# Performance work log

Measured on AMD Instinct MI355X. Metric: run time of the kernel, lower is better.

## Reference

```python
import jax, jax.numpy as jnp
import numpy as np

B, N, E, F, C = 4, 10000, 160000, 128, 128
NUM_ITERATIONS = 3  # num_iterations init arg


def setup_inputs() -> dict:
    key = jax.random.key(0)
    ks = jax.random.split(key, 8)
    objects = jax.random.normal(ks[0], (B, N, F), dtype=jnp.float32)
    connections = jax.random.randint(ks[1], (B, E, 2), 0, N, dtype=jnp.int32)
    # small init scales keep exp() in the attention numerically tame (mirrors
    # glorot/orthogonal-scale weights at init)
    object_state_W = jax.random.normal(ks[2], (F, C), dtype=jnp.float32) * (1.0 / np.sqrt(F))
    state_attention_W = jax.random.normal(ks[3], (C, C), dtype=jnp.float32) * 0.05
    linked_state_attention_W = jax.random.normal(ks[4], (C, C), dtype=jnp.float32) * 0.05
    linked_state_W = jax.random.normal(ks[5], (C, C), dtype=jnp.float32) * (1.0 / np.sqrt(C))
    attention_b = jnp.zeros((C,), dtype=jnp.float32)
    state_b = jnp.zeros((C,), dtype=jnp.float32)
    return {
        "objects": objects,
        "object_state_W": object_state_W,
        "state_attention_W": state_attention_W,
        "linked_state_attention_W": linked_state_attention_W,
        "attention_b": attention_b,
        "linked_state_W": linked_state_W,
        "state_b": state_b,
        "connections": connections,
    }


def reference(objects, object_state_W, state_attention_W, linked_state_attention_W,
              attention_b, linked_state_W, state_b, connections):
    # bidirectional: double edges with both orientations  [B, 2E]
    src = jnp.concatenate([connections[:, :, 0], connections[:, :, 1]], axis=1)
    dst = jnp.concatenate([connections[:, :, 1], connections[:, :, 0]], axis=1)

    # initial states: [B, N, C]
    states = jnp.tanh(jnp.einsum('bnf,fc->bnc', objects, object_state_W) + state_b)

    def step_one(states_b, src_b, dst_b):
        # states_b: [N, C]; src_b/dst_b: [2E]
        states_aW = states_b @ state_attention_W          # [N, C]
        linked_aW = states_b @ linked_state_attention_W   # [N, C]
        # per-edge unnormalized attention  [2E, C]
        attention = jnp.exp(states_aW[src_b] + linked_aW[dst_b] + attention_b)
        # scatter-add normalization; self edge contributes 1 (exp(0))
        attention_norm = jnp.ones_like(states_b).at[src_b].add(attention)  # [N, C]
        self_attention = 1.0 / attention_norm
        attention = attention / attention_norm[src_b]
        # weighted neighbor aggregation
        attented = attention * states_b[dst_b]                              # [2E, C]
        linked_gated = jnp.zeros_like(states_b).at[src_b].add(attented)     # [N, C]
        return jnp.tanh(states_b * self_attention + linked_gated @ linked_state_W + state_b)

    step = jax.vmap(step_one)
    for _ in range(NUM_ITERATIONS):
        states = step(states, src, dst)
    return states
```

## Files before the change

### kernel.cpp

```cpp
#include <hip/hip_runtime.h>
#include <hip/hip_bf16.h>


#define BATCH 4
#define NNODE 10000
#define NEDGE 160000
#define TWOE  (2*NEDGE)
#define MROWS (BATCH*NNODE)
#define NCHUNK 64
#define CHUNKE (NEDGE/NCHUNK)
#define PADN  10240
#define EDPAD (TWOE + 8*NNODE)

typedef unsigned short u16;
typedef unsigned int   u32;
typedef __attribute__((ext_vector_type(8))) short bf16x8_t;
typedef __attribute__((ext_vector_type(4))) float f32x4_t;

__device__ __forceinline__ float b2f(u16 h){ return __uint_as_float(((u32)h) << 16); }
__device__ __forceinline__ u16 f2bf(float f){
  u32 u = __float_as_uint(f);
  return (u16)((u + 0x7fffu + ((u >> 16) & 1u)) >> 16);
}
__device__ __forceinline__ float fast_tanh(float x){
  float e = __expf(2.0f * x);
  return fmaf(-2.0f, __builtin_amdgcn_rcpf(e + 1.0f), 1.0f);
}

__global__ void detect_dtype(const u32* __restrict__ objw, int* __restrict__ flag){
  __shared__ int zc, hc;
  if (threadIdx.x == 0){ zc = 0; hc = 0; }
  __syncthreads();
  int z = 0, h = 0;
  for (int i = threadIdx.x; i < 1024; i += 256){
    u32 lo = objw[i] & 0xffffu;
    if (lo == 0) z++;
    if (((lo >> 7) & 0xffu) >= 160u) h++;
  }
  atomicAdd(&zc, z); atomicAdd(&hc, h);
  __syncthreads();
  if (threadIdx.x == 0) *flag = (hc > 0 || zc > 512) ? 1 : 0;
}

__global__ void prep_weights(const void* __restrict__ Wo, const void* __restrict__ Wa,
                             const void* __restrict__ Wla, const void* __restrict__ Wl,
                             const void* __restrict__ ab, const void* __restrict__ sb,
                             const int* __restrict__ flag, u16* __restrict__ Wt,
                             float* __restrict__ biasf){
  int idx = blockIdx.x * 256 + threadIdx.x;
  bool f = (*flag != 0);
  if (idx < 65536){
    int m = idx >> 14, k = (idx >> 7) & 127, c = idx & 127;
    const void* src = (m == 0) ? Wo : (m == 1) ? Wa : (m == 2) ? Wla : Wl;
    u16 h = f ? f2bf(((const float*)src)[k * 128 + c]) : ((const u16*)src)[k * 128 + c];
    Wt[m * 16384 + c * 128 + k] = h;
  } else {
    int t = idx - 65536;
    const void* src = (t < 128) ? sb : ab;
    int i = t & 127;
    biasf[t] = f ? ((const float*)src)[i] : b2f(((const u16*)src)[i]);
  }
}

__device__ __forceinline__ void chunk_of(int blk, int& b, int& c){
  int xcd = blk & 7;
  b = xcd >> 1;
  c = ((blk >> 3) << 1) | (xcd & 1);
}

__global__ void __launch_bounds__(256) csr_hist(const int* __restrict__ conn,
                                                u16* __restrict__ partial){
  int b, c; chunk_of(blockIdx.x, b, c);
  __shared__ u32 hist[NNODE];
  for (int n = threadIdx.x; n < NNODE; n += 256) hist[n] = 0;
  __syncthreads();
  const int2* cp = (const int2*)conn + (size_t)b * NEDGE + c * CHUNKE;
  for (int i = threadIdx.x; i < CHUNKE; i += 256){
    int2 e = cp[i];
    atomicAdd(&hist[e.x], 1);
    atomicAdd(&hist[e.y], 1);
  }
  __syncthreads();
  u16* prow = partial + (size_t)(b * NCHUNK + c) * PADN;
  for (int n = threadIdx.x; n < NNODE; n += 256) prow[n] = (u16)hist[n];
}

__global__ void __launch_bounds__(256) csr_colscan(u16* __restrict__ partial,
    int* __restrict__ row_start, int* __restrict__ bsum, int* __restrict__ deg){
  int b = blockIdx.x / 40, w = blockIdx.x % 40;
  int n = w * 256 + threadIdx.x;
  u32 run = 0;
  if (n < NNODE){
    #pragma unroll 8
    for (int c = 0; c < NCHUNK; c++){
      size_t idx = (size_t)(b * NCHUNK + c) * PADN + n;
      u32 v = partial[idx];
      partial[idx] = (u16)run;
      run += v;
    }
  }
  u32 pad = (run + 7u) & ~7u;
  __shared__ u32 buf[256];
  buf[threadIdx.x] = pad;
  __syncthreads();
  for (int off = 1; off < 256; off <<= 1){
    u32 x = (threadIdx.x >= (unsigned)off) ? buf[threadIdx.x - off] : 0;
    __syncthreads();
    buf[threadIdx.x] += x;
    __syncthreads();
  }
  u32 incl = buf[threadIdx.x];
  if (n < NNODE){
    row_start[b * (NNODE + 1) + n] = (int)(incl - pad);
    deg[b * NNODE + n] = (int)run;
  }
  if (threadIdx.x == 255) bsum[blockIdx.x] = (int)incl;
}

__global__ void scanB(const int* __restrict__ bsum, int* __restrict__ boff,
                      int* __restrict__ row_start){
  __shared__ int s[160];
  if (threadIdx.x < 160) s[threadIdx.x] = bsum[threadIdx.x];
  __syncthreads();
  if (threadIdx.x < 160){
    int b = threadIdx.x / 40, j = threadIdx.x % 40;
    int off = 0;
    for (int q = b * 40; q < b * 40 + j; q++) off += s[q];
    boff[threadIdx.x] = off;
  }
  if (threadIdx.x < BATCH){
    int tot = 0;
    for (int q = threadIdx.x * 40; q < threadIdx.x * 40 + 40; q++) tot += s[q];
    row_start[threadIdx.x * (NNODE + 1) + NNODE] = tot;
  }
}

__global__ void scanC(int* __restrict__ row_start, const int* __restrict__ boff){
  int b = blockIdx.x / 40, j = blockIdx.x % 40;
  int n = j * 256 + threadIdx.x;
  if (n < NNODE) row_start[b * (NNODE + 1) + n] += boff[blockIdx.x];
}

__global__ void __launch_bounds__(256) csr_fill(const int* __restrict__ conn,
    const u16* __restrict__ partial, const int* __restrict__ row_start,
    int* __restrict__ edge_dst){
  int b, c; chunk_of(blockIdx.x, b, c);
  __shared__ u32 cur[NNODE];
  const u16* prow = partial + (size_t)(b * NCHUNK + c) * PADN;
  const int* rs = row_start + b * (NNODE + 1);
  for (int n = threadIdx.x; n < NNODE; n += 256) cur[n] = (u32)rs[n] + prow[n];
  __syncthreads();
  const int2* cp = (const int2*)conn + (size_t)b * NEDGE + c * CHUNKE;
  int* edb = edge_dst + (size_t)b * EDPAD;
  for (int i = threadIdx.x; i < CHUNKE; i += 256){
    int2 e = cp[i];
    u32 p1 = atomicAdd(&cur[e.x], 1); edb[p1] = e.y;
    u32 p2 = atomicAdd(&cur[e.y], 1); edb[p2] = e.x;
  }
}

__global__ void pad_fill(const int* __restrict__ row_start,
                         const int* __restrict__ deg, int* __restrict__ edge_dst){
  int b = blockIdx.x / 40, j = blockIdx.x % 40;
  int n = j * 256 + threadIdx.x;
  if (n >= NNODE) return;
  const int* rs = row_start + b * (NNODE + 1);
  int s = rs[n] + deg[b * NNODE + n];
  int epad = rs[n + 1];
  int sent = 40000 - 9999 * b;
  int* edb = edge_dst + (size_t)b * EDPAD;
  for (int p = s; p < epad; p++) edb[p] = sent;
}

__global__ void zero_sent(u32* __restrict__ g0, u32* __restrict__ g1){
  size_t base = (size_t)MROWS * 64;
  g0[base + threadIdx.x] = 0;
  g1[base + threadIdx.x] = 0;
}

__device__ __forceinline__ void gemm_tile4(const u16* __restrict__ arow,
    const u16* __restrict__ wt, int lm, int lq, int cofs, f32x4_t acc[4]){
  #pragma unroll
  for (int ks = 0; ks < 4; ks++){
    bf16x8_t a = *(const bf16x8_t*)(arow + ks * 32);
    #pragma unroll
    for (int nb = 0; nb < 4; nb++){
      bf16x8_t bfr = *(const bf16x8_t*)(wt + (cofs + nb * 16 + lm) * 128 + ks * 32 + lq * 8);
      acc[nb] = __builtin_amdgcn_mfma_f32_16x16x32_bf16(a, bfr, acc[nb], 0, 0, 0);
    }
  }
}

__device__ __forceinline__ void gemm_tile4_packed(const u32* __restrict__ Lrow,
    const u16* __restrict__ wt, int lm, int lq, int cofs, f32x4_t acc[4]){
  #pragma unroll
  for (int ks = 0; ks < 4; ks++){
    uint4 wa = *(const uint4*)(Lrow + ks * 32 + lq * 8);
    uint4 wb = *(const uint4*)(Lrow + ks * 32 + lq * 8 + 4);
    bf16x8_t a;
    a[0] = (short)wa.x; a[1] = (short)wa.y; a[2] = (short)wa.z; a[3] = (short)wa.w;
    a[4] = (short)wb.x; a[5] = (short)wb.y; a[6] = (short)wb.z; a[7] = (short)wb.w;
    #pragma unroll
    for (int nb = 0; nb < 4; nb++){
      bf16x8_t bfr = *(const bf16x8_t*)(wt + (cofs + nb * 16 + lm) * 128 + ks * 32 + lq * 8);
      acc[nb] = __builtin_amdgcn_mfma_f32_16x16x32_bf16(a, bfr, acc[nb], 0, 0, 0);
    }
  }
}

__device__ __forceinline__ void phase2_awlaw4(const u16* __restrict__ ldstile,
    const u16* __restrict__ Wt, const float* __restrict__ biasf,
    int lm, int lq, int cofs, int r0, _Float16* __restrict__ eat,
    u32* __restrict__ ghw){
  const u16* Wta  = Wt + 16384;
  const u16* Wtla = Wt + 32768;
  const u16* ldsrow = ldstile + lm * 136 + lq * 8;
  f32x4_t accA[4], accL[4];
  #pragma unroll
  for (int i = 0; i < 4; i++){ accA[i] = (f32x4_t){0.f,0.f,0.f,0.f}; accL[i] = (f32x4_t){0.f,0.f,0.f,0.f}; }
  #pragma unroll
  for (int ks = 0; ks < 4; ks++){
    bf16x8_t a = *(const bf16x8_t*)(ldsrow + ks * 32);
    #pragma unroll
    for (int nb = 0; nb < 4; nb++){
      bf16x8_t ba = *(const bf16x8_t*)(Wta  + (cofs + nb * 16 + lm) * 128 + ks * 32 + lq * 8);
      bf16x8_t bl = *(const bf16x8_t*)(Wtla + (cofs + nb * 16 + lm) * 128 + ks * 32 + lq * 8);
      accA[nb] = __builtin_amdgcn_mfma_f32_16x16x32_bf16(a, ba, accA[nb], 0, 0, 0);
      accL[nb] = __builtin_amdgcn_mfma_f32_16x16x32_bf16(a, bl, accL[nb], 0, 0, 0);
    }
  }
  #pragma unroll
  for (int nb = 0; nb < 4; nb++){
    int col = cofs + nb * 16 + lm;
    float bb = biasf[128 + col];
    #pragma unroll
    for (int i = 0; i < 4; i++){
      int row = r0 + lq * 4 + i;
      float ea = fminf(__expf(accA[nb][i]), 60000.0f);
      eat[(lq * 4 + i) * 128 + col] = (_Float16)ea;
      _Float16 elh = (_Float16)fminf(__expf(accL[nb][i] + bb), 60000.0f);
      u16 sbf = ldstile[(lq * 4 + i) * 136 + col];
      _Float16 sh = (_Float16)b2f(sbf);
      u32 elu = (u32)(*(const u16*)&elh);
      u32 shu = (u32)(*(const u16*)&sh);
      ghw[(size_t)row * 64 + (col & 63)] = elu | (shu << 16);
    }
  }
}

__device__ __forceinline__ void eah_writeback(const _Float16* __restrict__ eat,
    _Float16* __restrict__ eah, int blk_r0, int tid){
  const uint4* src = (const uint4*)eat;
  uint4* dst = (uint4*)(eah + (size_t)blk_r0 * 128);
  dst[tid]       = src[tid];
  dst[tid + 256] = src[tid + 256];
}

__global__ void __launch_bounds__(256) fused_init(const void* __restrict__ obj_raw,
    const int* __restrict__ flag, const u16* __restrict__ Wt,
    const float* __restrict__ biasf, _Float16* __restrict__ eah,
    u32* __restrict__ gat0, u32* __restrict__ gat1){
  __shared__ u16 lds[2][16 * 136];
  __shared__ _Float16 eat[2][16 * 128];
  const int lane = threadIdx.x & 63, wave = threadIdx.x >> 6;
  const int t = wave >> 1, ch = wave & 1, cofs = ch * 64;
  const int r0 = blockIdx.x * 32 + t * 16;
  const int lm = lane & 15, lq = lane >> 4;
  f32x4_t acc[4];
  #pragma unroll
  for (int i = 0; i < 4; i++) acc[i] = (f32x4_t){0.f, 0.f, 0.f, 0.f};
  if (*flag){
    const float* arow = (const float*)obj_raw + (size_t)(r0 + lm) * 128 + lq * 8;
    #pragma unroll
    for (int ks = 0; ks < 4; ks++){
      float4 fa = *(const float4*)(arow + ks * 32);
      float4 fb = *(const float4*)(arow + ks * 32 + 4);
      bf16x8_t a;
      a[0] = (short)f2bf(fa.x); a[1] = (short)f2bf(fa.y);
      a[2] = (short)f2bf(fa.z); a[3] = (short)f2bf(fa.w);
      a[4] = (short)f2bf(fb.x); a[5] = (short)f2bf(fb.y);
      a[6] = (short)f2bf(fb.z); a[7] = (short)f2bf(fb.w);
      #pragma unroll
      for (int nb = 0; nb < 4; nb++){
        bf16x8_t bfr = *(const bf16x8_t*)(Wt + (cofs + nb * 16 + lm) * 128 + ks * 32 + lq * 8);
        acc[nb] = __builtin_amdgcn_mfma_f32_16x16x32_bf16(a, bfr, acc[nb], 0, 0, 0);
      }
    }
  } else {
    gemm_tile4((const u16*)obj_raw + (size_t)(r0 + lm) * 128 + lq * 8, Wt, lm, lq, cofs, acc);
  }
  #pragma unroll
  for (int nb = 0; nb < 4; nb++){
    int col = cofs + nb * 16 + lm;
    float bb = biasf[col];
    #pragma unroll
    for (int i = 0; i < 4; i++)
      lds[t][(lq * 4 + i) * 136 + col] = f2bf(fast_tanh(acc[nb][i] + bb));
  }
  __syncthreads();
  phase2_awlaw4(&lds[t][0], Wt, biasf, lm, lq, cofs, r0, &eat[t][0], ch ? gat1 : gat0);
  __syncthreads();
  eah_writeback(&eat[0][0], eah, blockIdx.x * 32, threadIdx.x);
}

__global__ void __launch_bounds__(256) fused_mid(const u32* __restrict__ lgsa,
    const u16* __restrict__ Wt, const float* __restrict__ biasf,
    _Float16* __restrict__ eah, u32* __restrict__ gat0, u32* __restrict__ gat1){
  __shared__ u16 lds[2][16 * 136];
  __shared__ _Float16 eat[2][16 * 128];
  const int lane = threadIdx.x & 63, wave = threadIdx.x >> 6;
  const int t = wave >> 1, ch = wave & 1, cofs = ch * 64;
  const int r0 = blockIdx.x * 32 + t * 16;
  const int lm = lane & 15, lq = lane >> 4;
  f32x4_t acc[4];
  #pragma unroll
  for (int i = 0; i < 4; i++) acc[i] = (f32x4_t){0.f, 0.f, 0.f, 0.f};
  gemm_tile4_packed(lgsa + (size_t)(r0 + lm) * 128, Wt + 49152, lm, lq, cofs, acc);
  #pragma unroll
  for (int nb = 0; nb < 4; nb++){
    int col = cofs + nb * 16 + lm;
    float bb = biasf[col];
    #pragma unroll
    for (int i = 0; i < 4; i++){
      int row = r0 + lq * 4 + i;
      u32 v = lgsa[(size_t)row * 128 + col];
      u16 hb = (u16)(v >> 16);
      float sa = (float)(*(const _Float16*)&hb);
      lds[t][(lq * 4 + i) * 136 + col] = f2bf(fast_tanh(sa + acc[nb][i] + bb));
    }
  }
  __syncthreads();
  phase2_awlaw4(&lds[t][0], Wt, biasf, lm, lq, cofs, r0, &eat[t][0], ch ? gat1 : gat0);
  __syncthreads();
  eah_writeback(&eat[0][0], eah, blockIdx.x * 32, threadIdx.x);
}

__global__ void __launch_bounds__(256) final_out(const u32* __restrict__ lgsa,
    const u16* __restrict__ Wt, const float* __restrict__ biasf,
    const int* __restrict__ flag, void* __restrict__ outp){
  const int lane = threadIdx.x & 63, wave = threadIdx.x >> 6;
  const int t = wave >> 1, ch = wave & 1, cofs = ch * 64;
  const int r0 = blockIdx.x * 32 + t * 16;
  const int lm = lane & 15, lq = lane >> 4;
  bool f32out = (*flag != 0);
  f32x4_t acc[4];
  #pragma unroll
  for (int i = 0; i < 4; i++) acc[i] = (f32x4_t){0.f, 0.f, 0.f, 0.f};
  gemm_tile4_packed(lgsa + (size_t)(r0 + lm) * 128, Wt + 49152, lm, lq, cofs, acc);
  #pragma unroll
  for (int nb = 0; nb < 4; nb++){
    int col = cofs + nb * 16 + lm;
    float bb = biasf[col];
    #pragma unroll
    for (int i = 0; i < 4; i++){
      int row = r0 + lq * 4 + i;
      u32 vv = lgsa[(size_t)row * 128 + col];
      u16 hb = (u16)(vv >> 16);
      float sa = (float)(*(const _Float16*)&hb);
      float v = fast_tanh(sa + acc[nb][i] + bb);
      if (f32out) ((float*)outp)[(size_t)row * 128 + col] = v;
      else        ((u16*)  outp)[(size_t)row * 128 + col] = f2bf(v);
    }
  }
}

__device__ __forceinline__ void acc_mix(u32 g, float one, float& a1, float& a2){
  asm("v_fma_mix_f32 %0, %2, %3, %0 op_sel:[0,0,0] op_sel_hi:[1,0,0]\n\t"
      "v_fma_mix_f32 %1, %2, %2, %1 op_sel:[0,1,0] op_sel_hi:[1,1,0]"
      : "+v"(a1), "+v"(a2)
      : "v"(g), "v"(one));
}

__device__ __forceinline__ u32 gath1(const u32* __restrict__ gh, int d, int c){
  const u32* p = (const u32*)((const char*)gh + ((size_t)(u32)d << 8));
  return p[c];
}

__global__ void __launch_bounds__(256, 8) edge_kernel(const _Float16* __restrict__ eah,
    const u32* __restrict__ gat0, const u32* __restrict__ gat1,
    const int* __restrict__ row_start, const int* __restrict__ edge_dst,
    u32* __restrict__ lgsa){
  int blk = blockIdx.x;
  int xcd = blk & 7;
  int b = xcd >> 1, h = xcd & 1;
  int i = blk >> 3;
  int n = i * 4 + (int)(threadIdx.x >> 6);
  int node = b * NNODE + n;
  int c = threadIdx.x & 63;
  const u32* gh = (h ? gat1 : gat0) + (size_t)b * NNODE * 64;
  int e0 = __builtin_amdgcn_readfirstlane(row_start[b * (NNODE + 1) + n]);
  int e1 = __builtin_amdgcn_readfirstlane(row_start[b * (NNODE + 1) + n + 1]);
  const int* ed = edge_dst + (size_t)b * EDPAD;

  float ea = (float)eah[(size_t)node * 128 + h * 64 + c];
  u32 self = gh[((size_t)n << 6) + c];
  const float one = 1.0f;

  float s1 = 0.f, s2 = 0.f, t1 = 0.f, t2 = 0.f;
  int ng = (e1 - e0) >> 3;
  if (ng){
    int dB[8]; u32 g[8], gn[8];
    int e = e0;
    { const int* ep = ed + e;
      #pragma unroll
      for (int j = 0; j < 8; j++) dB[j] = __builtin_amdgcn_readfirstlane(ep[j]); }
    #pragma unroll
    for (int j = 0; j < 8; j++) g[j] = gath1(gh, dB[j], c);
    e += 8;
    { const int* ep = ed + e;
      #pragma unroll
      for (int j = 0; j < 8; j++) dB[j] = __builtin_amdgcn_readfirstlane(ep[j]); }
    e += 8;
    int k = 1;
    for (; k + 1 < ng; k += 2){
      #pragma unroll
      for (int j = 0; j < 8; j++) gn[j] = gath1(gh, dB[j], c);
      { const int* ep = ed + e;
        #pragma unroll
        for (int j = 0; j < 8; j++) dB[j] = __builtin_amdgcn_readfirstlane(ep[j]); }
      e += 8;
      #pragma unroll
      for (int j = 0; j < 8; j++) acc_mix(g[j], one, (j & 1) ? t1 : s1, (j & 1) ? t2 : s2);
      #pragma unroll
      for (int j = 0; j < 8; j++) g[j] = gath1(gh, dB[j], c);
      { const int* ep = ed + e;
        #pragma unroll
        for (int j = 0; j < 8; j++) dB[j] = __builtin_amdgcn_readfirstlane(ep[j]); }
      e += 8;
      #pragma unroll
      for (int j = 0; j < 8; j++) acc_mix(gn[j], one, (j & 1) ? t1 : s1, (j & 1) ? t2 : s2);
    }
    if (k < ng){
      #pragma unroll
      for (int j = 0; j < 8; j++) gn[j] = gath1(gh, dB[j], c);
      #pragma unroll
      for (int j = 0; j < 8; j++) acc_mix(g[j], one, (j & 1) ? t1 : s1, (j & 1) ? t2 : s2);
      #pragma unroll
      for (int j = 0; j < 8; j++) acc_mix(gn[j], one, (j & 1) ? t1 : s1, (j & 1) ? t2 : s2);
    } else {
      #pragma unroll
      for (int j = 0; j < 8; j++) acc_mix(g[j], one, (j & 1) ? t1 : s1, (j & 1) ? t2 : s2);
    }
  }

  s1 += t1; s2 += t2;
  float inv = __builtin_amdgcn_rcpf(fmaf(ea, s1, 1.0f));
  float lg = ea * s2 * inv;
  u16 hb = (u16)(self >> 16);
  float s_self = (float)(*(const _Float16*)&hb);
  _Float16 hs = (_Float16)(s_self * inv);
  u32 pk = (u32)f2bf(lg) | ((u32)(*(const u16*)&hs) << 16);
  lgsa[(size_t)node * 128 + h * 64 + c] = pk;
}

extern "C" void kernel_launch(void* const* d_in, const int* in_sizes, int n_in,
                              void* d_out, int out_size, void* d_ws, size_t ws_size,
                              hipStream_t stream){
  (void)in_sizes; (void)n_in; (void)ws_size; (void)out_size;
  const void* objects = d_in[0];
  const void* Wo      = d_in[1];
  const void* Wa      = d_in[2];
  const void* Wla     = d_in[3];
  const void* attn_b  = d_in[4];
  const void* Wl      = d_in[5];
  const void* state_b = d_in[6];
  const int*  conn    = (const int*)d_in[7];

  char* base = (char*)d_ws;
  size_t off = 0;
  auto alloc = [&](size_t bytes) -> char* {
    char* p = base + off;
    off = (off + bytes + 255) & ~(size_t)255;
    return p;
  };
  int*      flag      = (int*)     alloc(256);
  u16*      Wt        = (u16*)     alloc((size_t)4 * 16384 * 2);
  float*    biasf     = (float*)   alloc(256 * 4);
  _Float16* eah       = (_Float16*)alloc((size_t)MROWS * 128 * 2);
  u32*      gat0      = (u32*)     alloc((size_t)(MROWS + 4) * 64 * 4);
  u32*      gat1      = (u32*)     alloc((size_t)(MROWS + 4) * 64 * 4);
  u32*      lgsa      = (u32*)     alloc((size_t)MROWS * 128 * 4);
  u16*      partial   = (u16*)     alloc((size_t)BATCH * NCHUNK * PADN * 2);
  int*      row_start = (int*)     alloc((size_t)BATCH * (NNODE + 1) * 4);
  int*      edge_dst  = (int*)     alloc((size_t)BATCH * EDPAD * 4);
  int*      deg       = (int*)     alloc((size_t)MROWS * 4);
  int*      bsum      = (int*)     alloc(160 * 4);
  int*      boff      = (int*)     alloc(160 * 4);

  detect_dtype<<<1, 256, 0, stream>>>((const u32*)objects, flag);
  prep_weights<<<257, 256, 0, stream>>>(Wo, Wa, Wla, Wl, attn_b, state_b, flag, Wt, biasf);

  csr_hist<<<256, 256, 0, stream>>>(conn, partial);
  csr_colscan<<<160, 256, 0, stream>>>(partial, row_start, bsum, deg);
  scanB<<<1, 256, 0, stream>>>(bsum, boff, row_start);
  scanC<<<160, 256, 0, stream>>>(row_start, boff);
  csr_fill<<<256, 256, 0, stream>>>(conn, partial, row_start, edge_dst);
  pad_fill<<<160, 256, 0, stream>>>(row_start, deg, edge_dst);
  zero_sent<<<1, 256, 0, stream>>>(gat0, gat1);

  fused_init<<<MROWS / 32, 256, 0, stream>>>(objects, flag, Wt, biasf, eah, gat0, gat1);
  edge_kernel<<<MROWS / 2, 256, 0, stream>>>(eah, gat0, gat1, row_start, edge_dst, lgsa);
  fused_mid<<<MROWS / 32, 256, 0, stream>>>(lgsa, Wt, biasf, eah, gat0, gat1);
  edge_kernel<<<MROWS / 2, 256, 0, stream>>>(eah, gat0, gat1, row_start, edge_dst, lgsa);
  fused_mid<<<MROWS / 32, 256, 0, stream>>>(lgsa, Wt, biasf, eah, gat0, gat1);
  edge_kernel<<<MROWS / 2, 256, 0, stream>>>(eah, gat0, gat1, row_start, edge_dst, lgsa);
  final_out<<<MROWS / 32, 256, 0, stream>>>(lgsa, Wt, biasf, flag, d_out);
}
```

Before: 359.1 us.

## Use 16-byte vector gathers with edge split across lane quarters

Edge aggregation now has each wavefront split into four 16-lane groups. Each group handles a different edge and each lane loads a 16-byte chunk (four channels) of the neighbor row, where before every lane loaded one 4-byte word per edge. The aim is fewer, wider memory instructions and no scalar readfirstlane loads of edge indices, since each group reads its own index. The cost is a cross-lane shuffle reduction of eight accumulators at the end and a final store done by only a quarter of the lanes.

Result: slower. 395.4 us (+10.1%).

```diff
diff --git a/kernel.cpp b/kernel.cpp
--- a/kernel.cpp
+++ b/kernel.cpp
@@ -371,10 +371,13 @@
       : "v"(g), "v"(one));
 }
 
-__device__ __forceinline__ u32 gath1(const u32* __restrict__ gh, int d, int c){
-  const u32* p = (const u32*)((const char*)gh + ((size_t)(u32)d << 8));
-  return p[c];
-}
+__device__ __forceinline__ uint4 gath4(const u32* __restrict__ gh, int d, int pofs){
+  return *(const uint4*)((const char*)gh + (((size_t)(u32)d) << 8) + pofs);
+}
+
+#define ACC4(G) \
+  acc_mix((G).x, one, s1a, s2a); acc_mix((G).y, one, s1b, s2b); \
+  acc_mix((G).z, one, s1c, s2c); acc_mix((G).w, one, s1d, s2d);
 
 __global__ void __launch_bounds__(256, 8) edge_kernel(const _Float16* __restrict__ eah,
     const u32* __restrict__ gat0, const u32* __restrict__ gat1,
@@ -386,71 +389,76 @@
   int i = blk >> 3;
   int n = i * 4 + (int)(threadIdx.x >> 6);
   int node = b * NNODE + n;
-  int c = threadIdx.x & 63;
+  int lane = threadIdx.x & 63;
+  int q = lane >> 4;
+  int p = lane & 15;
+  int pofs = p << 4;
   const u32* gh = (h ? gat1 : gat0) + (size_t)b * NNODE * 64;
   int e0 = __builtin_amdgcn_readfirstlane(row_start[b * (NNODE + 1) + n]);
   int e1 = __builtin_amdgcn_readfirstlane(row_start[b * (NNODE + 1) + n + 1]);
-  const int* ed = edge_dst + (size_t)b * EDPAD;
-
-  float ea = (float)eah[(size_t)node * 128 + h * 64 + c];
-  u32 self = gh[((size_t)n << 6) + c];
+  const int* edq = edge_dst + (size_t)b * EDPAD + q;
+
+  uint2 eav = ((const uint2*)(eah + (size_t)node * 128 + h * 64))[p];
+  uint4 self4 = *(const uint4*)((const char*)gh + (((size_t)(u32)n) << 8) + pofs);
   const float one = 1.0f;
 
-  float s1 = 0.f, s2 = 0.f, t1 = 0.f, t2 = 0.f;
+  float s1a=0.f, s1b=0.f, s1c=0.f, s1d=0.f;
+  float s2a=0.f, s2b=0.f, s2c=0.f, s2d=0.f;
   int ng = (e1 - e0) >> 3;
   if (ng){
-    int dB[8]; u32 g[8], gn[8];
+    uint4 gA, gB, hA, hB;
+    int dA, dB;
     int e = e0;
-    { const int* ep = ed + e;
-      #pragma unroll
-      for (int j = 0; j < 8; j++) dB[j] = __builtin_amdgcn_readfirstlane(ep[j]); }
-    #pragma unroll
-    for (int j = 0; j < 8; j++) g[j] = gath1(gh, dB[j], c);
+    dA = edq[e]; dB = edq[e + 4];
+    gA = gath4(gh, dA, pofs); gB = gath4(gh, dB, pofs);
     e += 8;
-    { const int* ep = ed + e;
-      #pragma unroll
-      for (int j = 0; j < 8; j++) dB[j] = __builtin_amdgcn_readfirstlane(ep[j]); }
+    dA = edq[e]; dB = edq[e + 4];
     e += 8;
     int k = 1;
     for (; k + 1 < ng; k += 2){
-      #pragma unroll
-      for (int j = 0; j < 8; j++) gn[j] = gath1(gh, dB[j], c);
-      { const int* ep = ed + e;
-        #pragma unroll
-        for (int j = 0; j < 8; j++) dB[j] = __builtin_amdgcn_readfirstlane(ep[j]); }
-      e += 8;
-      #pragma unroll
-      for (int j = 0; j < 8; j++) acc_mix(g[j], one, (j & 1) ? t1 : s1, (j & 1) ? t2 : s2);
-      #pragma unroll
-      for (int j = 0; j < 8; j++) g[j] = gath1(gh, dB[j], c);
-      { const int* ep = ed + e;
-        #pragma unroll
-        for (int j = 0; j < 8; j++) dB[j] = __builtin_amdgcn_readfirstlane(ep[j]); }
-      e += 8;
-      #pragma unroll
-      for (int j = 0; j < 8; j++) acc_mix(gn[j], one, (j & 1) ? t1 : s1, (j & 1) ? t2 : s2);
+      hA = gath4(gh, dA, pofs); hB = gath4(gh, dB, pofs);
+      dA = edq[e]; dB = edq[e + 4]; e += 8;
+      ACC4(gA); ACC4(gB);
+      gA = gath4(gh, dA, pofs); gB = gath4(gh, dB, pofs);
+      dA = edq[e]; dB = edq[e + 4]; e += 8;
+      ACC4(hA); ACC4(hB);
     }
     if (k < ng){
-      #pragma unroll
-      for (int j = 0; j < 8; j++) gn[j] = gath1(gh, dB[j], c);
-      #pragma unroll
-      for (int j = 0; j < 8; j++) acc_mix(g[j], one, (j & 1) ? t1 : s1, (j & 1) ? t2 : s2);
-      #pragma unroll
-      for (int j = 0; j < 8; j++) acc_mix(gn[j], one, (j & 1) ? t1 : s1, (j & 1) ? t2 : s2);
+      hA = gath4(gh, dA, pofs); hB = gath4(gh, dB, pofs);
+      ACC4(gA); ACC4(gB);
+      ACC4(hA); ACC4(hB);
     } else {
-      #pragma unroll
-      for (int j = 0; j < 8; j++) acc_mix(g[j], one, (j & 1) ? t1 : s1, (j & 1) ? t2 : s2);
-    }
-  }
-
-  s1 += t1; s2 += t2;
-  float inv = __builtin_amdgcn_rcpf(fmaf(ea, s1, 1.0f));
-  float lg = ea * s2 * inv;
-  u16 hb = (u16)(self >> 16);
-  float s_self = (float)(*(const _Float16*)&hb);
-  _Float16 hs = (_Float16)(s_self * inv);
-  u32 pk = (u32)f2bf(lg) | ((u32)(*(const u16*)&hs) << 16);
-  lgsa[(size_t)node * 128 + h * 64 + c] = pk;
+      ACC4(gA); ACC4(gB);
+    }
+  }
+
+  s1a += __shfl_xor(s1a, 16, 64); s1a += __shfl_xor(s1a, 32, 64);
+  s1b += __shfl_xor(s1b, 16, 64); s1b += __shfl_xor(s1b, 32, 64);
+  s1c += __shfl_xor(s1c, 16, 64); s1c += __shfl_xor(s1c, 32, 64);
+  s1d += __shfl_xor(s1d, 16, 64); s1d += __shfl_xor(s1d, 32, 64);
+  s2a += __shfl_xor(s2a, 16, 64); s2a += __shfl_xor(s2a, 32, 64);
+  s2b += __shfl_xor(s2b, 16, 64); s2b += __shfl_xor(s2b, 32, 64);
+  s2c += __shfl_xor(s2c, 16, 64); s2c += __shfl_xor(s2c, 32, 64);
+  s2d += __shfl_xor(s2d, 16, 64); s2d += __shfl_xor(s2d, 32, 64);
+
+  if (q == 0){
+    union { uint2 u; _Float16 f[4]; } ec; ec.u = eav;
+    union { uint4 u; u32 w[4]; } sv; sv.u = self4;
+    float S1[4] = {s1a, s1b, s1c, s1d};
+    float S2[4] = {s2a, s2b, s2c, s2d};
+    u32 out[4];
+    #pragma unroll
+    for (int k2 = 0; k2 < 4; k2++){
+      float ea = (float)ec.f[k2];
+      float inv = __builtin_amdgcn_rcpf(fmaf(ea, S1[k2], 1.0f));
+      float lg = ea * S2[k2] * inv;
+      u16 hb = (u16)(sv.w[k2] >> 16);
+      float s_self = (float)(*(const _Float16*)&hb);
+      _Float16 hs = (_Float16)(s_self * inv);
+      out[k2] = (u32)f2bf(lg) | ((u32)(*(const u16*)&hs) << 16);
+    }
+    *(uint4*)(lgsa + (size_t)node * 128 + h * 64 + (p << 2)) = *(const uint4*)out;
+  }
 }
 
 extern "C" void kernel_launch(void* const* d_in, const int* in_sizes, int n_in,
```
